# Optimization experiments

Hardware: AMD Instinct MI355X
Metric: run time of the kernel (lower is better)

Reference implementation:

```python
import jax, jax.numpy as jnp
import numpy as np

NEG_INF = -1e30  # underflows to exactly 0 after softmax in fp32, matching -inf masking


def setup_inputs() -> dict:
    key = jax.random.key(0)
    k1, k2, k3, k4, k5, k6 = jax.random.split(key, 6)
    B, T, D = 4, 4096, 2048
    P, Lmax, c = 1024, 8, 128
    h = jax.random.normal(k1, (B, T, D), dtype=jnp.float32)
    phrase_mask = jax.random.randint(k2, (B, P, Lmax), 0, 2) > 0
    phrase_token_idx = jax.random.randint(k3, (B, P, Lmax), 0, T)
    W_kv = jax.random.normal(k4, (c, D), dtype=jnp.float32) * 0.02
    W_z = jax.random.normal(k5, (c, D), dtype=jnp.float32) * 0.02
    B_pos = jax.random.normal(k6, (Lmax, c), dtype=jnp.float32) * 0.02
    return {"h": h, "phrase_mask": phrase_mask, "phrase_token_idx": phrase_token_idx,
            "W_kv": W_kv, "W_z": W_z, "B_pos": B_pos}


def reference(h, phrase_mask, phrase_token_idx, W_kv, W_z, B_pos):
    B, P, Lmax = phrase_mask.shape
    D = h.shape[-1]
    # Gather phrase tokens: (B, P, Lmax, D)
    idx_flat = phrase_token_idx.reshape(B, P * Lmax)
    h_phrase = jnp.take_along_axis(h, idx_flat[:, :, None], axis=1).reshape(B, P, Lmax, D)
    # Dual thin projections (D -> c)
    c_tok = jnp.einsum('bpld,cd->bplc', h_phrase, W_kv)
    z_tok = jnp.einsum('bpld,cd->bplc', h_phrase, W_z) + B_pos[None, None, :, :]
    # Masked softmax over the phrase-slot dim Lmax
    z_masked = jnp.where(phrase_mask[..., None], z_tok, NEG_INF)
    gates = jax.nn.softmax(z_masked, axis=2)
    any_token = jnp.any(phrase_mask, axis=2)[:, :, None, None]
    gates = jnp.where(any_token, gates, 0.0)
    # Weighted reduce over slots -> (B, P, c)
    return jnp.sum(gates * c_tok, axis=2)
```

## Files before the change

kernel.cpp:

```cpp
#include <hip/hip_runtime.h>
#include <hip/hip_bf16.h>

#define DIM   2048
#define NC    256
#define CDIM  128
#define HALFCZ (16384u * 256u)

typedef __attribute__((ext_vector_type(8))) short short8;
typedef __attribute__((ext_vector_type(4))) float f32x4;

static __device__ __forceinline__ unsigned short f2bf(float f) {
    union { float f; unsigned u; } v; v.f = f;
    return (unsigned short)((v.u + 0x7fffu + ((v.u >> 16) & 1u)) >> 16);
}

static __device__ __forceinline__ short8 cvt8(float4 a, float4 b) {
    union { __hip_bfloat162 h2[4]; short8 s; } u;
    u.h2[0] = __float22bfloat162_rn(float2{a.x, a.y});
    u.h2[1] = __float22bfloat162_rn(float2{a.z, a.w});
    u.h2[2] = __float22bfloat162_rn(float2{b.x, b.y});
    u.h2[3] = __float22bfloat162_rn(float2{b.z, b.w});
    return u.s;
}

__global__ __launch_bounds__(256) void convert_w(const float* __restrict__ Wkv,
                                                 const float* __restrict__ Wz,
                                                 unsigned short* __restrict__ Wp) {
    int tid = blockIdx.x * 256 + threadIdx.x;
    int l = tid & 63;
    int s = (tid >> 6) & 63;
    int f = tid >> 12;
    int n = f * 16 + (l & 15);
    int k = s * 32 + ((l >> 4) << 3);
    const float* src = (n < CDIM) ? (Wkv + (size_t)n * DIM + k)
                                  : (Wz + (size_t)(n - CDIM) * DIM + k);
    float4 f0 = *(const float4*)src;
    float4 f1 = *(const float4*)(src + 4);
    *(short8*)(Wp + (size_t)tid * 8) = cvt8(f0, f1);
}

__global__ __launch_bounds__(256) void gemm_hw(
    const float* __restrict__ H,
    const unsigned short* __restrict__ Wp,
    float* __restrict__ CZp)
{
    __shared__ unsigned char As[2 * 64 * 128];

    const int tid    = threadIdx.x;
    const int lane   = tid & 63;
    const int wave   = tid >> 6;
    const int wn     = wave * 64;
    const int bid    = blockIdx.x;
    const int kslice = bid & 1;
    const int m0     = (bid >> 1) * 64;

    float* CZout = CZp + (size_t)kslice * HALFCZ;

    const int srow  = tid >> 2;
    const int scolf = (tid & 3) * 16;
    const float* gA = H + (size_t)(m0 + srow) * DIM + kslice * 1024 + scolf;
    const int swz   = (srow & 7) << 4;
    const int soff0 = (srow * 128 + scolf * 2) ^ swz;
    const int soff1 = (srow * 128 + scolf * 2 + 16) ^ swz;

    const unsigned short* wpb = Wp + (size_t)(wave * 4) * 32768 + lane * 8;

    f32x4 acc[4][4] = {};
    float4 p0[4], p1[4];
    short8 b0[2][4], b1[2][4];

#define LOADA(P, KT) { \
    _Pragma("unroll") \
    for (int q = 0; q < 4; ++q) P[q] = *(const float4*)(gA + (KT) * 64 + q * 4); }

#define LOADB(B, KT) { \
    _Pragma("unroll") \
    for (int ks = 0; ks < 2; ++ks) \
        _Pragma("unroll") \
        for (int j = 0; j < 4; ++j) \
            B[ks][j] = *(const short8*)(wpb + (size_t)j * 32768 + ((kslice << 5) + (KT) * 2 + ks) * 512); }

#define WRITES(BUFB, P) { \
    short8 lo_ = cvt8(P[0], P[1]); \
    short8 hi_ = cvt8(P[2], P[3]); \
    *(short8*)(As + (BUFB) + soff0) = lo_; \
    *(short8*)(As + (BUFB) + soff1) = hi_; }

#define COMPUTE(BUFB, B) { \
    _Pragma("unroll") \
    for (int ks = 0; ks < 2; ++ks) { \
        short8 a_[4]; \
        _Pragma("unroll") \
        for (int i = 0; i < 4; ++i) { \
            int row_ = i * 16 + (lane & 15); \
            int off_ = (row_ * 128 + ks * 64 + ((lane >> 4) << 4)) ^ ((row_ & 7) << 4); \
            a_[i] = *(const short8*)(As + (BUFB) + off_); \
        } \
        _Pragma("unroll") \
        for (int i = 0; i < 4; ++i) \
            _Pragma("unroll") \
            for (int j = 0; j < 4; ++j) \
                acc[i][j] = __builtin_amdgcn_mfma_f32_16x16x32_bf16(a_[i], B[ks][j], acc[i][j], 0, 0, 0); \
    } }

    LOADA(p0, 0);
    LOADB(b0, 0);
    WRITES(0, p0);
    LOADA(p1, 1);
    __syncthreads();

    for (int it = 0; it < 16; it += 2) {
        LOADB(b1, it + 1);
        WRITES(8192, p1);
        if (it + 2 < 16) LOADA(p0, it + 2);
        COMPUTE(0, b0);
        __syncthreads();

        if (it + 2 < 16) { LOADB(b0, it + 2); WRITES(0, p0); }
        if (it + 3 < 16) LOADA(p1, it + 3);
        COMPUTE(8192, b1);
        __syncthreads();
    }

    #pragma unroll
    for (int i = 0; i < 4; ++i)
        #pragma unroll
        for (int j = 0; j < 4; ++j)
            #pragma unroll
            for (int r = 0; r < 4; ++r) {
                int row = m0 + i * 16 + (lane >> 4) * 4 + r;
                int col = wn + j * 16 + (lane & 15);
                CZout[(size_t)row * NC + col] = acc[i][j][r];
            }
#undef LOADA
#undef LOADB
#undef WRITES
#undef COMPUTE
}

__global__ __launch_bounds__(256) void finalize(
    const float* __restrict__ CZp,
    const int*   __restrict__ mask,
    const int*   __restrict__ idx,
    const float* __restrict__ Bpos,
    float*       __restrict__ out)
{
    const float* CZ0 = CZp;
    const float* CZ1 = CZp + HALFCZ;

    int t  = threadIdx.x;
    int ch = t & 127;
    int q  = blockIdx.x * 2 + (t >> 7);
    int b  = q >> 10;

    int rows[8];
    unsigned mbits = 0;
    #pragma unroll
    for (int l = 0; l < 8; ++l) {
        int m   = mask[q * 8 + l];
        int tok = idx[q * 8 + l];
        rows[l] = b * 4096 + tok;
        if (m) mbits |= 1u << l;
    }

    float z[8], c[8];
    float mx = -1e30f;
    #pragma unroll
    for (int l = 0; l < 8; ++l) {
        if (mbits & (1u << l)) {
            size_t base = (size_t)rows[l] * NC;
            z[l] = CZ0[base + CDIM + ch] + CZ1[base + CDIM + ch] + Bpos[l * CDIM + ch];
            c[l] = CZ0[base + ch] + CZ1[base + ch];
            mx = fmaxf(mx, z[l]);
        } else {
            z[l] = -1e30f; c[l] = 0.f;
        }
    }

    float num = 0.f, den = 0.f;
    #pragma unroll
    for (int l = 0; l < 8; ++l) {
        if (mbits & (1u << l)) {
            float w = __expf(z[l] - mx);
            den += w;
            num += w * c[l];
        }
    }
    out[(size_t)q * CDIM + ch] = mbits ? (num / den) : 0.f;
}

extern "C" void kernel_launch(void* const* d_in, const int* in_sizes, int n_in,
                              void* d_out, int out_size, void* d_ws, size_t ws_size,
                              hipStream_t stream) {
    const float* h    = (const float*)d_in[0];
    const int*   mask = (const int*)d_in[1];
    const int*   idx  = (const int*)d_in[2];
    const float* Wkv  = (const float*)d_in[3];
    const float* Wz   = (const float*)d_in[4];
    const float* Bpos = (const float*)d_in[5];
    float* out = (float*)d_out;

    unsigned short* Wp = (unsigned short*)d_ws;
    float* CZp = (float*)((char*)d_ws + 2 * 1024 * 1024);

    convert_w<<<256, 256, 0, stream>>>(Wkv, Wz, Wp);
    gemm_hw<<<512, 256, 0, stream>>>(h, Wp, CZp);
    finalize<<<2048, 256, 0, stream>>>(CZp, mask, idx, Bpos, out);
}
```

Measured before the change: 47.24 us.

## Store GEMM partial projections as bf16 and tune barrier and MFMA priority

The GEMM now writes its split-K partial projection outputs as bf16 instead of fp32, which halves the intermediate write and the later gather traffic in finalize. Finalize widens the bf16 values back to fp32 before summing. __syncthreads is replaced by a custom LDS-wait-plus-barrier, all A fragments are loaded before the MFMA block, and the MFMA block runs at raised wave priority. The cost is lost precision in the partial sums: rounding each K-half to bf16 adds error to the logits and values.

```diff
diff --git a/kernel.cpp b/kernel.cpp
--- a/kernel.cpp
+++ b/kernel.cpp
@@ -12,6 +12,9 @@
 static __device__ __forceinline__ unsigned short f2bf(float f) {
     union { float f; unsigned u; } v; v.f = f;
     return (unsigned short)((v.u + 0x7fffu + ((v.u >> 16) & 1u)) >> 16);
+}
+static __device__ __forceinline__ float bf2f(unsigned short u) {
+    union { unsigned u; float f; } v; v.u = ((unsigned)u) << 16; return v.f;
 }
 
 static __device__ __forceinline__ short8 cvt8(float4 a, float4 b) {
@@ -22,6 +25,9 @@
     u.h2[3] = __float22bfloat162_rn(float2{b.z, b.w});
     return u.s;
 }
+
+#define BARRIER() { asm volatile("s_waitcnt lgkmcnt(0)" ::: "memory"); \
+                    __builtin_amdgcn_s_barrier(); }
 
 __global__ __launch_bounds__(256) void convert_w(const float* __restrict__ Wkv,
                                                  const float* __restrict__ Wz,
@@ -42,7 +48,7 @@
 __global__ __launch_bounds__(256) void gemm_hw(
     const float* __restrict__ H,
     const unsigned short* __restrict__ Wp,
-    float* __restrict__ CZp)
+    unsigned short* __restrict__ CZp)
 {
     __shared__ unsigned char As[2 * 64 * 128];
 
@@ -54,7 +60,7 @@
     const int kslice = bid & 1;
     const int m0     = (bid >> 1) * 64;
 
-    float* CZout = CZp + (size_t)kslice * HALFCZ;
+    unsigned short* CZout = CZp + (size_t)kslice * HALFCZ;
 
     const int srow  = tid >> 2;
     const int scolf = (tid & 3) * 16;
@@ -87,39 +93,42 @@
     *(short8*)(As + (BUFB) + soff1) = hi_; }
 
 #define COMPUTE(BUFB, B) { \
-    _Pragma("unroll") \
-    for (int ks = 0; ks < 2; ++ks) { \
-        short8 a_[4]; \
+    short8 a_[2][4]; \
+    _Pragma("unroll") \
+    for (int ks = 0; ks < 2; ++ks) \
         _Pragma("unroll") \
         for (int i = 0; i < 4; ++i) { \
             int row_ = i * 16 + (lane & 15); \
             int off_ = (row_ * 128 + ks * 64 + ((lane >> 4) << 4)) ^ ((row_ & 7) << 4); \
-            a_[i] = *(const short8*)(As + (BUFB) + off_); \
+            a_[ks][i] = *(const short8*)(As + (BUFB) + off_); \
         } \
+    __builtin_amdgcn_s_setprio(1); \
+    _Pragma("unroll") \
+    for (int ks = 0; ks < 2; ++ks) \
         _Pragma("unroll") \
         for (int i = 0; i < 4; ++i) \
             _Pragma("unroll") \
             for (int j = 0; j < 4; ++j) \
-                acc[i][j] = __builtin_amdgcn_mfma_f32_16x16x32_bf16(a_[i], B[ks][j], acc[i][j], 0, 0, 0); \
-    } }
+                acc[i][j] = __builtin_amdgcn_mfma_f32_16x16x32_bf16(a_[ks][i], B[ks][j], acc[i][j], 0, 0, 0); \
+    __builtin_amdgcn_s_setprio(0); }
 
     LOADA(p0, 0);
     LOADB(b0, 0);
     WRITES(0, p0);
     LOADA(p1, 1);
-    __syncthreads();
+    BARRIER();
 
     for (int it = 0; it < 16; it += 2) {
         LOADB(b1, it + 1);
         WRITES(8192, p1);
         if (it + 2 < 16) LOADA(p0, it + 2);
         COMPUTE(0, b0);
-        __syncthreads();
+        BARRIER();
 
         if (it + 2 < 16) { LOADB(b0, it + 2); WRITES(0, p0); }
         if (it + 3 < 16) LOADA(p1, it + 3);
         COMPUTE(8192, b1);
-        __syncthreads();
+        BARRIER();
     }
 
     #pragma unroll
@@ -130,7 +139,7 @@
             for (int r = 0; r < 4; ++r) {
                 int row = m0 + i * 16 + (lane >> 4) * 4 + r;
                 int col = wn + j * 16 + (lane & 15);
-                CZout[(size_t)row * NC + col] = acc[i][j][r];
+                CZout[(size_t)row * NC + col] = f2bf(acc[i][j][r]);
             }
 #undef LOADA
 #undef LOADB
@@ -139,14 +148,14 @@
 }
 
 __global__ __launch_bounds__(256) void finalize(
-    const float* __restrict__ CZp,
+    const unsigned short* __restrict__ CZp,
     const int*   __restrict__ mask,
     const int*   __restrict__ idx,
     const float* __restrict__ Bpos,
     float*       __restrict__ out)
 {
-    const float* CZ0 = CZp;
-    const float* CZ1 = CZp + HALFCZ;
+    const unsigned short* CZ0 = CZp;
+    const unsigned short* CZ1 = CZp + HALFCZ;
 
     int t  = threadIdx.x;
     int ch = t & 127;
@@ -169,8 +178,9 @@
     for (int l = 0; l < 8; ++l) {
         if (mbits & (1u << l)) {
             size_t base = (size_t)rows[l] * NC;
-            z[l] = CZ0[base + CDIM + ch] + CZ1[base + CDIM + ch] + Bpos[l * CDIM + ch];
-            c[l] = CZ0[base + ch] + CZ1[base + ch];
+            z[l] = bf2f(CZ0[base + CDIM + ch]) + bf2f(CZ1[base + CDIM + ch])
+                 + Bpos[l * CDIM + ch];
+            c[l] = bf2f(CZ0[base + ch]) + bf2f(CZ1[base + ch]);
             mx = fmaxf(mx, z[l]);
         } else {
             z[l] = -1e30f; c[l] = 0.f;
@@ -200,8 +210,8 @@
     const float* Bpos = (const float*)d_in[5];
     float* out = (float*)d_out;
 
-    unsigned short* Wp = (unsigned short*)d_ws;
-    float* CZp = (float*)((char*)d_ws + 2 * 1024 * 1024);
+    unsigned short* Wp  = (unsigned short*)d_ws;
+    unsigned short* CZp = (unsigned short*)((char*)d_ws + 2 * 1024 * 1024);
 
     convert_w<<<256, 256, 0, stream>>>(Wkv, Wz, Wp);
     gemm_hw<<<512, 256, 0, stream>>>(h, Wp, CZp);
```

Result: faster. 43.91 us (-7.0%).
